# Performance work log

Hardware: AMD Instinct MI355X
Metric: run time of the kernel (lower is better)

Reference implementation:

```python
import jax, jax.numpy as jnp
import numpy as np

N = 50000        # nodes
E = 800000       # edges per meta-path (avg degree 16)
M = 3            # meta-paths
IN = 256         # in_size
HID = 16         # hidden_size (per-head out dim of GATConv)
HEADS = 8
OUT = 8          # out_size (classes)
SA_HID = 128     # StructureAttention hidden_size default
NEG_SLOPE = 0.2  # DGL GATConv leaky_relu default


def setup_inputs() -> dict:
    key = jax.random.key(0)
    ks = jax.random.split(key, 11)
    h = jax.random.normal(ks[0], (N, IN), jnp.float32)
    edges = jax.random.randint(ks[1], (M, 2, E), 0, N, jnp.int32)  # [M, (src,dst), E]
    s = 0.05
    fc_w = jax.random.normal(ks[2], (M, IN, HEADS * HID), jnp.float32) * s
    attn_l = jax.random.normal(ks[3], (M, HEADS, HID), jnp.float32) * s
    attn_r = jax.random.normal(ks[4], (M, HEADS, HID), jnp.float32) * s
    sa_w1 = jax.random.normal(ks[5], (HEADS * HID, SA_HID), jnp.float32) * s
    sa_b1 = jnp.zeros((SA_HID,), jnp.float32)
    sa_w2 = jax.random.normal(ks[6], (SA_HID, 1), jnp.float32) * s
    pred_w = jax.random.normal(ks[7], (HEADS * HID, OUT), jnp.float32) * s
    pred_b = jnp.zeros((OUT,), jnp.float32)
    return {"h": h, "edges": edges, "fc_w": fc_w, "attn_l": attn_l,
            "attn_r": attn_r, "sa_w1": sa_w1, "sa_b1": sa_b1, "sa_w2": sa_w2,
            "pred_w": pred_w, "pred_b": pred_b}


def _gat(h, src, dst, w, al, ar):
    # DGL GATConv, eval mode (dropout=0), activation=elu
    feat = (h @ w).reshape(N, HEADS, HID)                 # [N,H,D]
    el = jnp.einsum('nhd,hd->nh', feat, al)               # [N,H]
    er = jnp.einsum('nhd,hd->nh', feat, ar)               # [N,H]
    e = el[src] + er[dst]                                 # [E,H]
    e = jnp.where(e > 0, e, NEG_SLOPE * e)                # leaky_relu
    # edge softmax over incoming edges of each dst node
    emax = jax.ops.segment_max(e, dst, num_segments=N)    # [N,H]
    ex = jnp.exp(e - emax[dst])                           # [E,H]
    denom = jax.ops.segment_sum(ex, dst, num_segments=N)  # [N,H]
    alpha = ex / denom[dst]                               # [E,H]
    msg = feat[src] * alpha[:, :, None]                   # [E,H,D]
    out = jax.ops.segment_sum(msg, dst, num_segments=N)   # [N,H,D]
    return jax.nn.elu(out).reshape(N, HEADS * HID)        # flatten(1)


def reference(h, edges, fc_w, attn_l, attn_r, sa_w1, sa_b1, sa_w2, pred_w, pred_b):
    # per-meta-path GAT (loop over fixed small set of meta-paths)
    zs = [_gat(h, edges[i, 0], edges[i, 1], fc_w[i], attn_l[i], attn_r[i])
          for i in range(M)]
    z = jnp.stack(zs, axis=1)                             # [N, M, H*D]
    # StructureAttention exactly as in source: softmax over dim 0 (nodes)
    w = jnp.tanh(z @ sa_w1 + sa_b1) @ sa_w2               # [N, M, 1]
    beta = jax.nn.softmax(w, axis=0)                      # softmax over nodes
    fused = (beta * z).sum(0)                             # [M, H*D]
    return fused @ pred_w + pred_b                        # [M, OUT]
```

## Files before the change

### kernel.cpp

```cpp
#include <hip/hip_runtime.h>

#define N_NODES 50000
#define N_EDGES 800000
#define N_META 3
#define IN_DIM 256
#define HD 128
#define HEADS 8
#define HID 16
#define OUT_DIM 8
#define NBKT 196
#define BCAP 5120
#define TILE_E 4096
#define NUMPAD 2064
#define GEMM_BX ((N_NODES + 63) / 64)
#define ELER_BX ((N_NODES * HEADS + 255) / 256)
#define BING_NB (3 * NBKT)

using bf16x8 = __attribute__((ext_vector_type(8))) short;
using f32x4  = __attribute__((ext_vector_type(4))) float;

__device__ __forceinline__ float bf2f(unsigned short u) {
  union { unsigned int i; float f; } x; x.i = ((unsigned int)u) << 16; return x.f;
}
__device__ __forceinline__ unsigned short f2bf(float f) {
  union { float f; unsigned int i; } x; x.f = f;
  unsigned int r = x.i + 0x7fffu + ((x.i >> 16) & 1u);
  return (unsigned short)(r >> 16);
}
__device__ __forceinline__ float tanh_fast(float x) {
  float e = __expf(2.f * x);
  return 1.f - 2.f / (e + 1.f);
}

__global__ __launch_bounds__(256)
void prep_kernel(const float* __restrict__ fcw, const float* __restrict__ w1,
                 unsigned short* __restrict__ fcwT, unsigned short* __restrict__ w1T,
                 float* __restrict__ numpad3, int* __restrict__ gcur) {
  int i = blockIdx.x * 256 + threadIdx.x;
  const int NFC = N_META * IN_DIM * HD;
  const int NW1 = HD * HD;
  const int NNP = N_META * NUMPAD;
  const int NGC = N_META * NBKT;
  if (i < NFC) {
    int p = i / (IN_DIM * HD);
    int rem = i - p * (IN_DIM * HD);
    int k = rem / HD, n = rem - k * HD;
    fcwT[(size_t)p * HD * IN_DIM + n * IN_DIM + k] = f2bf(fcw[i]);
  } else if (i < NFC + NW1) {
    int j = i - NFC;
    int k = j / HD, n = j - k * HD;
    w1T[n * HD + k] = f2bf(w1[j]);
  } else if (i < NFC + NW1 + NNP) {
    numpad3[i - NFC - NW1] = 0.f;
  } else if (i < NFC + NW1 + NNP + NGC) {
    gcur[i - NFC - NW1 - NNP] = 0;
  }
}

__global__ __launch_bounds__(256)
void bin_gemm_kernel(const int* __restrict__ edges, int* __restrict__ gcur,
                     unsigned int* __restrict__ bktbuf,
                     const float* __restrict__ A,
                     const unsigned short* __restrict__ BT,
                     unsigned short* __restrict__ Cb, int nrows) {
  __shared__ char smem[35840];
  int t = threadIdx.x;
  int bx = blockIdx.x;
  if (bx < BING_NB) {
    int p = bx / NBKT;
    int b = bx - p * NBKT;
    int* hist  = (int*)smem;
    int* gbase = hist + NBKT;
    int* fill  = gbase + NBKT;
    int e0 = b * TILE_E;
    const int* src = edges + (size_t)p * 2 * N_EDGES;
    const int* dst = src + N_EDGES;
    for (int i = t; i < NBKT; i += 256) { hist[i] = 0; fill[i] = 0; }
    __syncthreads();
    for (int i = t; i < TILE_E; i += 256) {
      int e = e0 + i;
      if (e < N_EDGES) atomicAdd(&hist[dst[e] >> 8], 1);
    }
    __syncthreads();
    for (int i = t; i < NBKT; i += 256) {
      int idx = p * NBKT + i;
      gbase[i] = hist[i] ? (idx * BCAP + atomicAdd(&gcur[idx], hist[i])) : 0;
    }
    __syncthreads();
    for (int i = t; i < TILE_E; i += 256) {
      int e = e0 + i;
      if (e < N_EDGES) {
        int d = dst[e];
        int b2 = d >> 8;
        int r = atomicAdd(&fill[b2], 1);
        bktbuf[gbase[b2] + r] = ((unsigned int)(d & 255) << 16) | (unsigned int)src[e];
      }
    }
  } else {
    unsigned short* As = (unsigned short*)smem;
    unsigned short* Bs = As + 64 * 40;
    int w = t >> 6, l = t & 63, q = l >> 4, s = l & 15;
    int row0 = (bx - BING_NB) * 64;
    f32x4 acc[3][8] = {};
    for (int k0 = 0; k0 < IN_DIM; k0 += 32) {
      {
        int r = t >> 2, c = (t & 3) * 8;
        int gr = row0 + r;
        float4 a0, a1;
        if (gr < nrows) {
          a0 = *(const float4*)(A + (size_t)gr * IN_DIM + k0 + c);
          a1 = *(const float4*)(A + (size_t)gr * IN_DIM + k0 + c + 4);
        } else {
          a0 = make_float4(0.f, 0.f, 0.f, 0.f); a1 = a0;
        }
        ushort4 u0, u1;
        u0.x = f2bf(a0.x); u0.y = f2bf(a0.y); u0.z = f2bf(a0.z); u0.w = f2bf(a0.w);
        u1.x = f2bf(a1.x); u1.y = f2bf(a1.y); u1.z = f2bf(a1.z); u1.w = f2bf(a1.w);
        *(ushort4*)&As[r * 40 + c]     = u0;
        *(ushort4*)&As[r * 40 + c + 4] = u1;
      }
      {
        int n = t >> 1, c = (t & 1) * 16;
        #pragma unroll
        for (int mm = 0; mm < 3; ++mm) {
          const unsigned short* BTm =
              BT + (size_t)mm * HD * IN_DIM + (size_t)n * IN_DIM + k0 + c;
          uint4 b0 = *(const uint4*)(BTm);
          uint4 b1 = *(const uint4*)(BTm + 8);
          unsigned short* Bsm = Bs + mm * (128 * 40) + n * 40 + c;
          *(uint4*)&Bsm[0] = b0;
          *(uint4*)&Bsm[8] = b1;
        }
      }
      __syncthreads();
      bf16x8 af = *(bf16x8*)&As[(w * 16 + s) * 40 + q * 8];
      #pragma unroll
      for (int mm = 0; mm < 3; ++mm) {
        #pragma unroll
        for (int f = 0; f < 8; ++f) {
          bf16x8 bfv = *(bf16x8*)&Bs[mm * (128 * 40) + (f * 16 + s) * 40 + q * 8];
          acc[mm][f] = __builtin_amdgcn_mfma_f32_16x16x32_bf16(af, bfv, acc[mm][f], 0, 0, 0);
        }
      }
      __syncthreads();
    }
    #pragma unroll
    for (int mm = 0; mm < 3; ++mm) {
      unsigned short* Cm = Cb + (size_t)mm * N_NODES * HD;
      #pragma unroll
      for (int f = 0; f < 8; ++f) {
        #pragma unroll
        for (int r = 0; r < 4; ++r) {
          int gr = row0 + w * 16 + q * 4 + r;
          if (gr < nrows) Cm[(size_t)gr * HD + f * 16 + s] = f2bf(acc[mm][f][r]);
        }
      }
    }
  }
}

__global__ __launch_bounds__(256)
void sort_eler_kernel(const int* __restrict__ gcur,
                      const unsigned int* __restrict__ bktbuf,
                      int* __restrict__ offsB, int* __restrict__ offsE,
                      int* __restrict__ csr,
                      const unsigned short* __restrict__ featb3,
                      const float* __restrict__ al, const float* __restrict__ ar,
                      float* __restrict__ el3, float* __restrict__ er3) {
  __shared__ int lh[256];
  __shared__ int cur[256];
  __shared__ int wsum[4];
  int p = blockIdx.y;
  int t = threadIdx.x;
  if (blockIdx.x < NBKT) {
    int b = blockIdx.x;
    int lane = t & 63, wid = t >> 6;
    int idx = p * NBKT + b;
    int S = idx * BCAP;
    int E = S + gcur[idx];
    int node0 = b * 256;
    int nn = min(256, N_NODES - node0);
    int gi0 = p * N_NODES + node0;
    lh[t] = 0;
    __syncthreads();
    for (int i = S + t; i < E; i += 256) atomicAdd(&lh[bktbuf[i] >> 16], 1);
    __syncthreads();
    int v = lh[t];
    int s = v;
    #pragma unroll
    for (int d = 1; d < 64; d <<= 1) {
      int x = __shfl_up(s, d);
      if (lane >= d) s += x;
    }
    if (lane == 63) wsum[wid] = s;
    __syncthreads();
    int woff = 0;
    #pragma unroll
    for (int k = 0; k < 4; ++k) if (k < wid) woff += wsum[k];
    int excl = S + woff + s - v;
    if (t < nn) {
      offsB[gi0 + t] = excl;
      offsE[gi0 + t] = excl + v;
    }
    cur[t] = excl;
    __syncthreads();
    for (int i = S + t; i < E; i += 256) {
      unsigned int rec = bktbuf[i];
      int pos = atomicAdd(&cur[rec >> 16], 1);
      csr[pos] = (int)(rec & 0xffffu);
    }
  } else {
    int i = (blockIdx.x - NBKT) * 256 + t;
    if (i >= N_NODES * HEADS) return;
    int node = i >> 3, hh = i & 7;
    const unsigned short* f =
        featb3 + (size_t)p * N_NODES * HD + (size_t)node * HD + hh * HID;
    uint4 u0 = *(const uint4*)(f);
    uint4 u1 = *(const uint4*)(f + 8);
    unsigned int uu[8] = {u0.x, u0.y, u0.z, u0.w, u1.x, u1.y, u1.z, u1.w};
    const float* alm = al + p * HD + hh * HID;
    const float* arm = ar + p * HD + hh * HID;
    float sl = 0.f, sr = 0.f;
    #pragma unroll
    for (int q = 0; q < 8; ++q) {
      float v0 = __uint_as_float(uu[q] << 16);
      float v1 = __uint_as_float(uu[q] & 0xffff0000u);
      int d = q * 2;
      sl += v0 * alm[d] + v1 * alm[d + 1];
      sr += v0 * arm[d] + v1 * arm[d + 1];
    }
    el3[(size_t)p * N_NODES * HEADS + i] = sl;
    er3[(size_t)p * N_NODES * HEADS + i] = sr;
  }
}

__global__ __launch_bounds__(256)
void aggregate_kernel(const int* __restrict__ offsB3, const int* __restrict__ offsE3,
                      const int* __restrict__ csr,
                      const uint4* __restrict__ featb3_u4,
                      const float* __restrict__ el3, const float* __restrict__ er3,
                      uint4* __restrict__ zb3_u4) {
  int m = blockIdx.y;
  int node = blockIdx.x * 4 + (threadIdx.x >> 6);
  if (node >= N_NODES) return;
  const uint4* featb_u4 = featb3_u4 + (size_t)m * N_NODES * 16;
  const float* el = el3 + (size_t)m * N_NODES * HEADS;
  const float* er = er3 + (size_t)m * N_NODES * HEADS;
  uint4* z_u4 = zb3_u4 + (size_t)m * N_NODES * 16;
  int lane = threadIdx.x & 63;
  int qg = lane >> 4;
  int li = lane & 15;
  int ch = li >> 1;
  int beg = offsB3[m * N_NODES + node], end = offsE3[m * N_NODES + node];
  float erh = er[node * HEADS + ch];
  float ssum = 0.f;
  float a[8] = {};
  for (int i = beg; i < end; i += 16) {
    int nk = end - i;
    int last = end - 1;
    int s0 = csr[min(i + qg,      last)];
    int s1 = csr[min(i + qg + 4,  last)];
    int s2 = csr[min(i + qg + 8,  last)];
    int s3 = csr[min(i + qg + 12, last)];
    uint4 v0 = featb_u4[(size_t)s0 * 16 + li];
    uint4 v1 = featb_u4[(size_t)s1 * 16 + li];
    uint4 v2 = featb_u4[(size_t)s2 * 16 + li];
    uint4 v3 = featb_u4[(size_t)s3 * 16 + li];
    float e0 = el[s0 * HEADS + ch] + erh;
    float e1 = el[s1 * HEADS + ch] + erh;
    float e2 = el[s2 * HEADS + ch] + erh;
    float e3 = el[s3 * HEADS + ch] + erh;
    e0 = e0 > 0.f ? e0 : 0.2f * e0;
    e1 = e1 > 0.f ? e1 : 0.2f * e1;
    e2 = e2 > 0.f ? e2 : 0.2f * e2;
    e3 = e3 > 0.f ? e3 : 0.2f * e3;
    float w0 = (qg      < nk) ? __expf(e0) : 0.f;
    float w1 = (qg + 4  < nk) ? __expf(e1) : 0.f;
    float w2 = (qg + 8  < nk) ? __expf(e2) : 0.f;
    float w3 = (qg + 12 < nk) ? __expf(e3) : 0.f;
    ssum += (w0 + w1) + (w2 + w3);
    a[0] += w0 * __uint_as_float(v0.x << 16);
    a[1] += w0 * __uint_as_float(v0.x & 0xffff0000u);
    a[2] += w0 * __uint_as_float(v0.y << 16);
    a[3] += w0 * __uint_as_float(v0.y & 0xffff0000u);
    a[4] += w0 * __uint_as_float(v0.z << 16);
    a[5] += w0 * __uint_as_float(v0.z & 0xffff0000u);
    a[6] += w0 * __uint_as_float(v0.w << 16);
    a[7] += w0 * __uint_as_float(v0.w & 0xffff0000u);
    a[0] += w1 * __uint_as_float(v1.x << 16);
    a[1] += w1 * __uint_as_float(v1.x & 0xffff0000u);
    a[2] += w1 * __uint_as_float(v1.y << 16);
    a[3] += w1 * __uint_as_float(v1.y & 0xffff0000u);
    a[4] += w1 * __uint_as_float(v1.z << 16);
    a[5] += w1 * __uint_as_float(v1.z & 0xffff0000u);
    a[6] += w1 * __uint_as_float(v1.w << 16);
    a[7] += w1 * __uint_as_float(v1.w & 0xffff0000u);
    a[0] += w2 * __uint_as_float(v2.x << 16);
    a[1] += w2 * __uint_as_float(v2.x & 0xffff0000u);
    a[2] += w2 * __uint_as_float(v2.y << 16);
    a[3] += w2 * __uint_as_float(v2.y & 0xffff0000u);
    a[4] += w2 * __uint_as_float(v2.z << 16);
    a[5] += w2 * __uint_as_float(v2.z & 0xffff0000u);
    a[6] += w2 * __uint_as_float(v2.w << 16);
    a[7] += w2 * __uint_as_float(v2.w & 0xffff0000u);
    a[0] += w3 * __uint_as_float(v3.x << 16);
    a[1] += w3 * __uint_as_float(v3.x & 0xffff0000u);
    a[2] += w3 * __uint_as_float(v3.y << 16);
    a[3] += w3 * __uint_as_float(v3.y & 0xffff0000u);
    a[4] += w3 * __uint_as_float(v3.z << 16);
    a[5] += w3 * __uint_as_float(v3.z & 0xffff0000u);
    a[6] += w3 * __uint_as_float(v3.w << 16);
    a[7] += w3 * __uint_as_float(v3.w & 0xffff0000u);
  }
  #pragma unroll
  for (int j = 0; j < 8; ++j) {
    a[j] += __shfl_xor(a[j], 16);
    a[j] += __shfl_xor(a[j], 32);
  }
  ssum += __shfl_xor(ssum, 16);
  ssum += __shfl_xor(ssum, 32);
  float inv = (end > beg) ? 1.f / ssum : 0.f;
  if (qg == 0) {
    #pragma unroll
    for (int j = 0; j < 8; ++j) {
      float z = a[j] * inv;
      a[j] = z > 0.f ? z : __expf(z) - 1.f;
    }
    uint4 o;
    unsigned int p0, p1, p2, p3;
    asm("v_cvt_pk_bf16_f32 %0, %1, %2" : "=v"(p0) : "v"(a[0]), "v"(a[1]));
    asm("v_cvt_pk_bf16_f32 %0, %1, %2" : "=v"(p1) : "v"(a[2]), "v"(a[3]));
    asm("v_cvt_pk_bf16_f32 %0, %1, %2" : "=v"(p2) : "v"(a[4]), "v"(a[5]));
    asm("v_cvt_pk_bf16_f32 %0, %1, %2" : "=v"(p3) : "v"(a[6]), "v"(a[7]));
    o.x = p0; o.y = p1; o.z = p2; o.w = p3;
    z_u4[(size_t)node * 16 + li] = o;
  }
}

__global__ __launch_bounds__(256)
void w_gemm_mfma(const unsigned short* __restrict__ Zb3,
                 const unsigned short* __restrict__ BT,
                 const float* __restrict__ B1, const float* __restrict__ W2,
                 float* __restrict__ numpad3, int nrows) {
  __shared__ unsigned short Bs[128 * 136];
  __shared__ unsigned short As[64 * 136];
  __shared__ float wrow[64];
  __shared__ float part[4][64][2];
  __shared__ float dpart[4];
  int tid = threadIdx.x;
  int m = blockIdx.y;
  const unsigned short* Zb = Zb3 + (size_t)m * N_NODES * HD;
  float* numpad = numpad3 + (size_t)m * NUMPAD;
  int w = tid >> 6, l = tid & 63, q = l >> 4, s = l & 15;
  {
    int n = tid >> 1, c0 = (tid & 1) * 64;
    #pragma unroll
    for (int j = 0; j < 8; ++j)
      *(uint4*)&Bs[n * 136 + c0 + j * 8] = *(const uint4*)(BT + n * HD + c0 + j * 8);
  }
  float b1v[8], w2v[8];
  #pragma unroll
  for (int f = 0; f < 8; ++f) { b1v[f] = B1[f * 16 + s]; w2v[f] = W2[f * 16 + s]; }
  float a0 = 0.f, a1 = 0.f, ld = 0.f;
  for (int t = 0; t < 4; ++t) {
    int row0 = blockIdx.x * 256 + t * 64;
    __syncthreads();
    {
      int r = tid >> 2, c0 = (tid & 3) * 32;
      int gr = row0 + r;
      if (gr < nrows) {
        #pragma unroll
        for (int j = 0; j < 4; ++j)
          *(uint4*)&As[r * 136 + c0 + j * 8] =
              *(const uint4*)(Zb + (size_t)gr * HD + c0 + j * 8);
      } else {
        uint4 z = make_uint4(0, 0, 0, 0);
        #pragma unroll
        for (int j = 0; j < 4; ++j) *(uint4*)&As[r * 136 + c0 + j * 8] = z;
      }
    }
    __syncthreads();
    f32x4 acc[8] = {};
    #pragma unroll
    for (int kc = 0; kc < 4; ++kc) {
      bf16x8 af = *(bf16x8*)&As[(w * 16 + s) * 136 + kc * 32 + q * 8];
      #pragma unroll
      for (int f = 0; f < 8; ++f) {
        bf16x8 bf = *(bf16x8*)&Bs[(f * 16 + s) * 136 + kc * 32 + q * 8];
        acc[f] = __builtin_amdgcn_mfma_f32_16x16x32_bf16(af, bf, acc[f], 0, 0, 0);
      }
    }
    #pragma unroll
    for (int r = 0; r < 4; ++r) {
      float p = 0.f;
      #pragma unroll
      for (int f = 0; f < 8; ++f) p += tanh_fast(acc[f][r] + b1v[f]) * w2v[f];
      p += __shfl_xor(p, 1); p += __shfl_xor(p, 2);
      p += __shfl_xor(p, 4); p += __shfl_xor(p, 8);
      if (s == 0) wrow[w * 16 + q * 4 + r] = p;
    }
    __syncthreads();
    for (int r = w; r < 64; r += 4) {
      int gr = row0 + r;
      if (gr < nrows) {
        float e = __expf(wrow[r]);
        unsigned int v = *(const unsigned int*)&As[r * 136 + 2 * l];
        a0 += e * __uint_as_float(v << 16);
        a1 += e * __uint_as_float(v & 0xffff0000u);
        if (l == 0) ld += e;
      }
    }
  }
  part[w][l][0] = a0;
  part[w][l][1] = a1;
  if (l == 0) dpart[w] = ld;
  __syncthreads();
  if (w == 0) {
    float s0 = part[0][l][0] + part[1][l][0] + part[2][l][0] + part[3][l][0];
    float s1 = part[0][l][1] + part[1][l][1] + part[2][l][1] + part[3][l][1];
    atomicAdd(&numpad[(2 * l) * 16], s0);
    atomicAdd(&numpad[(2 * l + 1) * 16], s1);
    if (l == 0)
      atomicAdd(&numpad[128 * 16], dpart[0] + dpart[1] + dpart[2] + dpart[3]);
  }
}

__global__ void final_kernel(const float* __restrict__ numpad,
                             const float* __restrict__ PW, const float* __restrict__ PB,
                             float* __restrict__ out) {
  int t = threadIdx.x;
  if (t >= N_META * OUT_DIM) return;
  int m = t >> 3, o = t & 7;
  const float* np = numpad + m * NUMPAD;
  float inv = 1.0f / np[128 * 16];
  float s = 0.f;
  for (int k = 0; k < HD; ++k) s += np[k * 16] * PW[k * OUT_DIM + o];
  out[t] = s * inv + PB[o];
}

extern "C" void kernel_launch(void* const* d_in, const int* in_sizes, int n_in,
                              void* d_out, int out_size, void* d_ws, size_t ws_size,
                              hipStream_t stream) {
  (void)in_sizes; (void)n_in; (void)out_size; (void)ws_size;
  const float* h     = (const float*)d_in[0];
  const int*   edges = (const int*)d_in[1];
  const float* fcw   = (const float*)d_in[2];
  const float* al    = (const float*)d_in[3];
  const float* ar    = (const float*)d_in[4];
  const float* w1    = (const float*)d_in[5];
  const float* b1    = (const float*)d_in[6];
  const float* w2    = (const float*)d_in[7];
  const float* pw    = (const float*)d_in[8];
  const float* pb    = (const float*)d_in[9];
  float* out = (float*)d_out;

  char* ws = (char*)d_ws;
  size_t off = 0;
  auto alloc = [&](size_t bytes) -> void* {
    void* p = ws + off;
    off = (off + bytes + 255) & ~(size_t)255;
    return p;
  };
  unsigned short* featb3 = (unsigned short*)alloc((size_t)N_META * N_NODES * HD * 2);
  unsigned short* zb3    = (unsigned short*)alloc((size_t)N_META * N_NODES * HD * 2);
  unsigned short* fcwT   = (unsigned short*)alloc((size_t)N_META * HD * IN_DIM * 2);
  unsigned short* w1T    = (unsigned short*)alloc((size_t)HD * HD * 2);
  float* el3 = (float*)alloc((size_t)N_META * N_NODES * HEADS * 4);
  float* er3 = (float*)alloc((size_t)N_META * N_NODES * HEADS * 4);
  int* gcur  = (int*)alloc((size_t)N_META * NBKT * 4);
  int* offsB = (int*)alloc((size_t)N_META * N_NODES * 4);
  int* offsE = (int*)alloc((size_t)N_META * N_NODES * 4);
  unsigned int* bktbuf = (unsigned int*)alloc((size_t)N_META * NBKT * BCAP * 4);
  int* csr   = (int*)alloc((size_t)N_META * NBKT * BCAP * 4);
  float* numpad = (float*)alloc((size_t)N_META * NUMPAD * 4);

  const int PREP_N = N_META * IN_DIM * HD + HD * HD + N_META * NUMPAD + N_META * NBKT;
  prep_kernel<<<(PREP_N + 255) / 256, 256, 0, stream>>>(
      fcw, w1, fcwT, w1T, numpad, gcur);

  bin_gemm_kernel<<<BING_NB + GEMM_BX, 256, 0, stream>>>(
      edges, gcur, bktbuf, h, fcwT, featb3, N_NODES);

  dim3 bgrid_(NBKT + ELER_BX, N_META);
  sort_eler_kernel<<<bgrid_, 256, 0, stream>>>(
      gcur, bktbuf, offsB, offsE, csr, featb3, al, ar, el3, er3);

  dim3 ggrid((N_NODES + 3) / 4, N_META);
  aggregate_kernel<<<ggrid, 256, 0, stream>>>(
      offsB, offsE, csr, (const uint4*)featb3, el3, er3, (uint4*)zb3);

  dim3 wgrid((N_NODES + 255) / 256, N_META);
  w_gemm_mfma<<<wgrid, 256, 0, stream>>>(zb3, w1T, b1, w2, numpad, N_NODES);

  final_kernel<<<1, 64, 0, stream>>>(numpad, pw, pb, out);
}
```

Baseline: 344.3 us.

## Fuse el/er attention scores into GEMM epilogue and split aggregation per meta-path

Computes the per-head el/er attention dot products directly from the GEMM accumulators, rounded to bf16 first to match the stored features, using lane shuffles. This removes the separate el/er pass that re-read the feature matrix from memory. The sort kernel becomes a pure CSR build, and aggregation is launched once per meta-path instead of as one 2D grid, which may improve cache locality per meta-path but adds launch overhead. The epilogue adds many shuffles and register pressure to the GEMM.

```diff
diff --git a/kernel.cpp b/kernel.cpp
--- a/kernel.cpp
+++ b/kernel.cpp
@@ -13,7 +13,6 @@
 #define TILE_E 4096
 #define NUMPAD 2064
 #define GEMM_BX ((N_NODES + 63) / 64)
-#define ELER_BX ((N_NODES * HEADS + 255) / 256)
 #define BING_NB (3 * NBKT)
 
 using bf16x8 = __attribute__((ext_vector_type(8))) short;
@@ -62,7 +61,10 @@
                      unsigned int* __restrict__ bktbuf,
                      const float* __restrict__ A,
                      const unsigned short* __restrict__ BT,
-                     unsigned short* __restrict__ Cb, int nrows) {
+                     unsigned short* __restrict__ Cb,
+                     const float* __restrict__ al, const float* __restrict__ ar,
+                     float* __restrict__ el3, float* __restrict__ er3,
+                     int nrows) {
   __shared__ char smem[35840];
   int t = threadIdx.x;
   int bx = blockIdx.x;
@@ -156,81 +158,84 @@
         }
       }
     }
+    #pragma unroll
+    for (int mm = 0; mm < 3; ++mm) {
+      float vel[4] = {0.f, 0.f, 0.f, 0.f};
+      float ver[4] = {0.f, 0.f, 0.f, 0.f};
+      #pragma unroll
+      for (int f = 0; f < 8; ++f) {
+        float av = al[mm * HD + f * 16 + s];
+        float aw = ar[mm * HD + f * 16 + s];
+        #pragma unroll
+        for (int r = 0; r < 4; ++r) {
+          float rv = bf2f(f2bf(acc[mm][f][r]));
+          float pl = rv * av, pr = rv * aw;
+          pl += __shfl_xor(pl, 1); pl += __shfl_xor(pl, 2);
+          pl += __shfl_xor(pl, 4); pl += __shfl_xor(pl, 8);
+          pr += __shfl_xor(pr, 1); pr += __shfl_xor(pr, 2);
+          pr += __shfl_xor(pr, 4); pr += __shfl_xor(pr, 8);
+          vel[r] = (s == 2 * f)     ? pl : vel[r];
+          ver[r] = (s == 2 * f + 1) ? pr : ver[r];
+        }
+      }
+      #pragma unroll
+      for (int r = 0; r < 4; ++r) {
+        int gr = row0 + w * 16 + q * 4 + r;
+        if (gr < nrows) {
+          size_t base = (size_t)mm * N_NODES * HEADS + (size_t)gr * HEADS + (s >> 1);
+          if (!(s & 1)) el3[base] = vel[r];
+          else          er3[base] = ver[r];
+        }
+      }
+    }
   }
 }
 
 __global__ __launch_bounds__(256)
-void sort_eler_kernel(const int* __restrict__ gcur,
-                      const unsigned int* __restrict__ bktbuf,
-                      int* __restrict__ offsB, int* __restrict__ offsE,
-                      int* __restrict__ csr,
-                      const unsigned short* __restrict__ featb3,
-                      const float* __restrict__ al, const float* __restrict__ ar,
-                      float* __restrict__ el3, float* __restrict__ er3) {
+void csr_kernel(const int* __restrict__ gcur,
+                const unsigned int* __restrict__ bktbuf,
+                int* __restrict__ offsB, int* __restrict__ offsE,
+                int* __restrict__ csr) {
   __shared__ int lh[256];
   __shared__ int cur[256];
   __shared__ int wsum[4];
   int p = blockIdx.y;
   int t = threadIdx.x;
-  if (blockIdx.x < NBKT) {
-    int b = blockIdx.x;
-    int lane = t & 63, wid = t >> 6;
-    int idx = p * NBKT + b;
-    int S = idx * BCAP;
-    int E = S + gcur[idx];
-    int node0 = b * 256;
-    int nn = min(256, N_NODES - node0);
-    int gi0 = p * N_NODES + node0;
-    lh[t] = 0;
-    __syncthreads();
-    for (int i = S + t; i < E; i += 256) atomicAdd(&lh[bktbuf[i] >> 16], 1);
-    __syncthreads();
-    int v = lh[t];
-    int s = v;
-    #pragma unroll
-    for (int d = 1; d < 64; d <<= 1) {
-      int x = __shfl_up(s, d);
-      if (lane >= d) s += x;
-    }
-    if (lane == 63) wsum[wid] = s;
-    __syncthreads();
-    int woff = 0;
-    #pragma unroll
-    for (int k = 0; k < 4; ++k) if (k < wid) woff += wsum[k];
-    int excl = S + woff + s - v;
-    if (t < nn) {
-      offsB[gi0 + t] = excl;
-      offsE[gi0 + t] = excl + v;
-    }
-    cur[t] = excl;
-    __syncthreads();
-    for (int i = S + t; i < E; i += 256) {
-      unsigned int rec = bktbuf[i];
-      int pos = atomicAdd(&cur[rec >> 16], 1);
-      csr[pos] = (int)(rec & 0xffffu);
-    }
-  } else {
-    int i = (blockIdx.x - NBKT) * 256 + t;
-    if (i >= N_NODES * HEADS) return;
-    int node = i >> 3, hh = i & 7;
-    const unsigned short* f =
-        featb3 + (size_t)p * N_NODES * HD + (size_t)node * HD + hh * HID;
-    uint4 u0 = *(const uint4*)(f);
-    uint4 u1 = *(const uint4*)(f + 8);
-    unsigned int uu[8] = {u0.x, u0.y, u0.z, u0.w, u1.x, u1.y, u1.z, u1.w};
-    const float* alm = al + p * HD + hh * HID;
-    const float* arm = ar + p * HD + hh * HID;
-    float sl = 0.f, sr = 0.f;
-    #pragma unroll
-    for (int q = 0; q < 8; ++q) {
-      float v0 = __uint_as_float(uu[q] << 16);
-      float v1 = __uint_as_float(uu[q] & 0xffff0000u);
-      int d = q * 2;
-      sl += v0 * alm[d] + v1 * alm[d + 1];
-      sr += v0 * arm[d] + v1 * arm[d + 1];
-    }
-    el3[(size_t)p * N_NODES * HEADS + i] = sl;
-    er3[(size_t)p * N_NODES * HEADS + i] = sr;
+  int b = blockIdx.x;
+  int lane = t & 63, wid = t >> 6;
+  int idx = p * NBKT + b;
+  int S = idx * BCAP;
+  int E = S + gcur[idx];
+  int node0 = b * 256;
+  int nn = min(256, N_NODES - node0);
+  int gi0 = p * N_NODES + node0;
+  lh[t] = 0;
+  __syncthreads();
+  for (int i = S + t; i < E; i += 256) atomicAdd(&lh[bktbuf[i] >> 16], 1);
+  __syncthreads();
+  int v = lh[t];
+  int s = v;
+  #pragma unroll
+  for (int d = 1; d < 64; d <<= 1) {
+    int x = __shfl_up(s, d);
+    if (lane >= d) s += x;
+  }
+  if (lane == 63) wsum[wid] = s;
+  __syncthreads();
+  int woff = 0;
+  #pragma unroll
+  for (int k = 0; k < 4; ++k) if (k < wid) woff += wsum[k];
+  int excl = S + woff + s - v;
+  if (t < nn) {
+    offsB[gi0 + t] = excl;
+    offsE[gi0 + t] = excl + v;
+  }
+  cur[t] = excl;
+  __syncthreads();
+  for (int i = S + t; i < E; i += 256) {
+    unsigned int rec = bktbuf[i];
+    int pos = atomicAdd(&cur[rec >> 16], 1);
+    csr[pos] = (int)(rec & 0xffffu);
   }
 }
 
@@ -239,8 +244,7 @@
                       const int* __restrict__ csr,
                       const uint4* __restrict__ featb3_u4,
                       const float* __restrict__ el3, const float* __restrict__ er3,
-                      uint4* __restrict__ zb3_u4) {
-  int m = blockIdx.y;
+                      uint4* __restrict__ zb3_u4, int m) {
   int node = blockIdx.x * 4 + (threadIdx.x >> 6);
   if (node >= N_NODES) return;
   const uint4* featb_u4 = featb3_u4 + (size_t)m * N_NODES * 16;
@@ -479,15 +483,15 @@
       fcw, w1, fcwT, w1T, numpad, gcur);
 
   bin_gemm_kernel<<<BING_NB + GEMM_BX, 256, 0, stream>>>(
-      edges, gcur, bktbuf, h, fcwT, featb3, N_NODES);
-
-  dim3 bgrid_(NBKT + ELER_BX, N_META);
-  sort_eler_kernel<<<bgrid_, 256, 0, stream>>>(
-      gcur, bktbuf, offsB, offsE, csr, featb3, al, ar, el3, er3);
-
-  dim3 ggrid((N_NODES + 3) / 4, N_META);
-  aggregate_kernel<<<ggrid, 256, 0, stream>>>(
-      offsB, offsE, csr, (const uint4*)featb3, el3, er3, (uint4*)zb3);
+      edges, gcur, bktbuf, h, fcwT, featb3, al, ar, el3, er3, N_NODES);
+
+  dim3 bgrid_(NBKT, N_META);
+  csr_kernel<<<bgrid_, 256, 0, stream>>>(gcur, bktbuf, offsB, offsE, csr);
+
+  for (int mm = 0; mm < N_META; ++mm) {
+    aggregate_kernel<<<(N_NODES + 3) / 4, 256, 0, stream>>>(
+        offsB, offsE, csr, (const uint4*)featb3, el3, er3, (uint4*)zb3, mm);
+  }
 
   dim3 wgrid((N_NODES + 255) / 256, N_META);
   w_gemm_mfma<<<wgrid, 256, 0, stream>>>(zb3, w1T, b1, w2, numpad, N_NODES);
```

New measurement: 415.5 us. 20.7% more time.

## Split bin/GEMM kernel, retile GEMM waves, launch aggregate per meta-path

Applied to the files above, without the earlier changes.

Splits the fused edge-binning and feature GEMM kernel into two separate launches. The GEMM gets a new wave tiling: each wave now covers all 64 rows and 96 of the 384 output columns, keeping its B fragments in registers and reusing them across four row tiles instead of reloading them. The aggregate kernel is now launched once per meta-path rather than as a single 2D grid. The intent is better register and LDS reuse in the GEMM and possibly better cache locality in aggregation, at the cost of extra launches and the loss of overlap between binning and GEMM.

```diff
diff --git a/kernel.cpp b/kernel.cpp
--- a/kernel.cpp
+++ b/kernel.cpp
@@ -58,102 +58,106 @@
 }
 
 __global__ __launch_bounds__(256)
-void bin_gemm_kernel(const int* __restrict__ edges, int* __restrict__ gcur,
-                     unsigned int* __restrict__ bktbuf,
-                     const float* __restrict__ A,
-                     const unsigned short* __restrict__ BT,
-                     unsigned short* __restrict__ Cb, int nrows) {
-  __shared__ char smem[35840];
+void bin_kernel(const int* __restrict__ edges, int* __restrict__ gcur,
+                unsigned int* __restrict__ bktbuf) {
+  __shared__ int hist[NBKT];
+  __shared__ int gbase[NBKT];
+  __shared__ int fill[NBKT];
   int t = threadIdx.x;
   int bx = blockIdx.x;
-  if (bx < BING_NB) {
-    int p = bx / NBKT;
-    int b = bx - p * NBKT;
-    int* hist  = (int*)smem;
-    int* gbase = hist + NBKT;
-    int* fill  = gbase + NBKT;
-    int e0 = b * TILE_E;
-    const int* src = edges + (size_t)p * 2 * N_EDGES;
-    const int* dst = src + N_EDGES;
-    for (int i = t; i < NBKT; i += 256) { hist[i] = 0; fill[i] = 0; }
-    __syncthreads();
-    for (int i = t; i < TILE_E; i += 256) {
-      int e = e0 + i;
-      if (e < N_EDGES) atomicAdd(&hist[dst[e] >> 8], 1);
-    }
-    __syncthreads();
-    for (int i = t; i < NBKT; i += 256) {
-      int idx = p * NBKT + i;
-      gbase[i] = hist[i] ? (idx * BCAP + atomicAdd(&gcur[idx], hist[i])) : 0;
-    }
-    __syncthreads();
-    for (int i = t; i < TILE_E; i += 256) {
-      int e = e0 + i;
-      if (e < N_EDGES) {
-        int d = dst[e];
-        int b2 = d >> 8;
-        int r = atomicAdd(&fill[b2], 1);
-        bktbuf[gbase[b2] + r] = ((unsigned int)(d & 255) << 16) | (unsigned int)src[e];
+  int p = bx / NBKT;
+  int b = bx - p * NBKT;
+  int e0 = b * TILE_E;
+  const int* src = edges + (size_t)p * 2 * N_EDGES;
+  const int* dst = src + N_EDGES;
+  for (int i = t; i < NBKT; i += 256) { hist[i] = 0; fill[i] = 0; }
+  __syncthreads();
+  for (int i = t; i < TILE_E; i += 256) {
+    int e = e0 + i;
+    if (e < N_EDGES) atomicAdd(&hist[dst[e] >> 8], 1);
+  }
+  __syncthreads();
+  for (int i = t; i < NBKT; i += 256) {
+    int idx = p * NBKT + i;
+    gbase[i] = hist[i] ? (idx * BCAP + atomicAdd(&gcur[idx], hist[i])) : 0;
+  }
+  __syncthreads();
+  for (int i = t; i < TILE_E; i += 256) {
+    int e = e0 + i;
+    if (e < N_EDGES) {
+      int d = dst[e];
+      int b2 = d >> 8;
+      int r = atomicAdd(&fill[b2], 1);
+      bktbuf[gbase[b2] + r] = ((unsigned int)(d & 255) << 16) | (unsigned int)src[e];
+    }
+  }
+}
+
+__global__ __launch_bounds__(256)
+void gemm_kernel(const float* __restrict__ A,
+                 const unsigned short* __restrict__ BT,
+                 unsigned short* __restrict__ Cb, int nrows) {
+  __shared__ unsigned short As[64 * 40];
+  __shared__ unsigned short Bs[384 * 40];
+  int t = threadIdx.x;
+  int w = t >> 6, l = t & 63, q = l >> 4, s = l & 15;
+  int row0 = blockIdx.x * 64;
+  f32x4 acc[4][6] = {};
+  for (int k0 = 0; k0 < IN_DIM; k0 += 32) {
+    {
+      int r = t >> 2, c = (t & 3) * 8;
+      int gr = row0 + r;
+      float4 a0, a1;
+      if (gr < nrows) {
+        a0 = *(const float4*)(A + (size_t)gr * IN_DIM + k0 + c);
+        a1 = *(const float4*)(A + (size_t)gr * IN_DIM + k0 + c + 4);
+      } else {
+        a0 = make_float4(0.f, 0.f, 0.f, 0.f); a1 = a0;
       }
-    }
-  } else {
-    unsigned short* As = (unsigned short*)smem;
-    unsigned short* Bs = As + 64 * 40;
-    int w = t >> 6, l = t & 63, q = l >> 4, s = l & 15;
-    int row0 = (bx - BING_NB) * 64;
-    f32x4 acc[3][8] = {};
-    for (int k0 = 0; k0 < IN_DIM; k0 += 32) {
-      {
-        int r = t >> 2, c = (t & 3) * 8;
-        int gr = row0 + r;
-        float4 a0, a1;
-        if (gr < nrows) {
-          a0 = *(const float4*)(A + (size_t)gr * IN_DIM + k0 + c);
-          a1 = *(const float4*)(A + (size_t)gr * IN_DIM + k0 + c + 4);
-        } else {
-          a0 = make_float4(0.f, 0.f, 0.f, 0.f); a1 = a0;
-        }
-        ushort4 u0, u1;
-        u0.x = f2bf(a0.x); u0.y = f2bf(a0.y); u0.z = f2bf(a0.z); u0.w = f2bf(a0.w);
-        u1.x = f2bf(a1.x); u1.y = f2bf(a1.y); u1.z = f2bf(a1.z); u1.w = f2bf(a1.w);
-        *(ushort4*)&As[r * 40 + c]     = u0;
-        *(ushort4*)&As[r * 40 + c + 4] = u1;
-      }
-      {
-        int n = t >> 1, c = (t & 1) * 16;
-        #pragma unroll
-        for (int mm = 0; mm < 3; ++mm) {
-          const unsigned short* BTm =
-              BT + (size_t)mm * HD * IN_DIM + (size_t)n * IN_DIM + k0 + c;
-          uint4 b0 = *(const uint4*)(BTm);
-          uint4 b1 = *(const uint4*)(BTm + 8);
-          unsigned short* Bsm = Bs + mm * (128 * 40) + n * 40 + c;
-          *(uint4*)&Bsm[0] = b0;
-          *(uint4*)&Bsm[8] = b1;
-        }
-      }
-      __syncthreads();
-      bf16x8 af = *(bf16x8*)&As[(w * 16 + s) * 40 + q * 8];
+      ushort4 u0, u1;
+      u0.x = f2bf(a0.x); u0.y = f2bf(a0.y); u0.z = f2bf(a0.z); u0.w = f2bf(a0.w);
+      u1.x = f2bf(a1.x); u1.y = f2bf(a1.y); u1.z = f2bf(a1.z); u1.w = f2bf(a1.w);
+      *(ushort4*)&As[r * 40 + c]     = u0;
+      *(ushort4*)&As[r * 40 + c + 4] = u1;
+    }
+    {
+      int n = t >> 1, c = (t & 1) * 16;
       #pragma unroll
       for (int mm = 0; mm < 3; ++mm) {
-        #pragma unroll
-        for (int f = 0; f < 8; ++f) {
-          bf16x8 bfv = *(bf16x8*)&Bs[mm * (128 * 40) + (f * 16 + s) * 40 + q * 8];
-          acc[mm][f] = __builtin_amdgcn_mfma_f32_16x16x32_bf16(af, bfv, acc[mm][f], 0, 0, 0);
-        }
+        const unsigned short* BTm =
+            BT + (size_t)mm * HD * IN_DIM + (size_t)n * IN_DIM + k0 + c;
+        uint4 b0 = *(const uint4*)(BTm);
+        uint4 b1 = *(const uint4*)(BTm + 8);
+        unsigned short* Bsm = Bs + (mm * 128 + n) * 40 + c;
+        *(uint4*)&Bsm[0] = b0;
+        *(uint4*)&Bsm[8] = b1;
       }
-      __syncthreads();
-    }
-    #pragma unroll
-    for (int mm = 0; mm < 3; ++mm) {
+    }
+    __syncthreads();
+    bf16x8 bfv[6];
+    #pragma unroll
+    for (int nt = 0; nt < 6; ++nt)
+      bfv[nt] = *(bf16x8*)&Bs[(w * 96 + nt * 16 + s) * 40 + q * 8];
+    #pragma unroll
+    for (int mt = 0; mt < 4; ++mt) {
+      bf16x8 af = *(bf16x8*)&As[(mt * 16 + s) * 40 + q * 8];
+      #pragma unroll
+      for (int nt = 0; nt < 6; ++nt)
+        acc[mt][nt] = __builtin_amdgcn_mfma_f32_16x16x32_bf16(af, bfv[nt], acc[mt][nt], 0, 0, 0);
+    }
+    __syncthreads();
+  }
+  #pragma unroll
+  for (int mt = 0; mt < 4; ++mt) {
+    #pragma unroll
+    for (int nt = 0; nt < 6; ++nt) {
+      int gc = w * 96 + nt * 16 + s;
+      int mm = gc >> 7, cim = gc & 127;
       unsigned short* Cm = Cb + (size_t)mm * N_NODES * HD;
       #pragma unroll
-      for (int f = 0; f < 8; ++f) {
-        #pragma unroll
-        for (int r = 0; r < 4; ++r) {
-          int gr = row0 + w * 16 + q * 4 + r;
-          if (gr < nrows) Cm[(size_t)gr * HD + f * 16 + s] = f2bf(acc[mm][f][r]);
-        }
+      for (int r = 0; r < 4; ++r) {
+        int gr = row0 + mt * 16 + q * 4 + r;
+        if (gr < nrows) Cm[(size_t)gr * HD + cim] = f2bf(acc[mt][nt][r]);
       }
     }
   }
@@ -239,8 +243,7 @@
                       const int* __restrict__ csr,
                       const uint4* __restrict__ featb3_u4,
                       const float* __restrict__ el3, const float* __restrict__ er3,
-                      uint4* __restrict__ zb3_u4) {
-  int m = blockIdx.y;
+                      uint4* __restrict__ zb3_u4, int m) {
   int node = blockIdx.x * 4 + (threadIdx.x >> 6);
   if (node >= N_NODES) return;
   const uint4* featb_u4 = featb3_u4 + (size_t)m * N_NODES * 16;
@@ -478,16 +481,17 @@
   prep_kernel<<<(PREP_N + 255) / 256, 256, 0, stream>>>(
       fcw, w1, fcwT, w1T, numpad, gcur);
 
-  bin_gemm_kernel<<<BING_NB + GEMM_BX, 256, 0, stream>>>(
-      edges, gcur, bktbuf, h, fcwT, featb3, N_NODES);
+  bin_kernel<<<BING_NB, 256, 0, stream>>>(edges, gcur, bktbuf);
+  gemm_kernel<<<GEMM_BX, 256, 0, stream>>>(h, fcwT, featb3, N_NODES);
 
   dim3 bgrid_(NBKT + ELER_BX, N_META);
   sort_eler_kernel<<<bgrid_, 256, 0, stream>>>(
       gcur, bktbuf, offsB, offsE, csr, featb3, al, ar, el3, er3);
 
-  dim3 ggrid((N_NODES + 3) / 4, N_META);
-  aggregate_kernel<<<ggrid, 256, 0, stream>>>(
-      offsB, offsE, csr, (const uint4*)featb3, el3, er3, (uint4*)zb3);
+  for (int mm = 0; mm < N_META; ++mm) {
+    aggregate_kernel<<<(N_NODES + 3) / 4, 256, 0, stream>>>(
+        offsB, offsE, csr, (const uint4*)featb3, el3, er3, (uint4*)zb3, mm);
+  }
 
   dim3 wgrid((N_NODES + 255) / 256, N_META);
   w_gemm_mfma<<<wgrid, 256, 0, stream>>>(zb3, w1T, b1, w2, numpad, N_NODES);
```

Result: slower. 363.0 us (+5.4%).
